# Kernel optimization log

Measured on AMD Instinct MI355X. Metric: run time of the kernel, lower is better.

The kernel has to match this reference:

```python
import jax, jax.numpy as jnp
import numpy as np

D_MODEL = 1024
N_HEAD = 16
D_HEAD = 64  # scale uses d_head even though heads are never split in this module
HD = N_HEAD * D_HEAD  # 1024
LN_EPS = 1e-5


def setup_inputs() -> dict:
    key = jax.random.key(0)
    ks = jax.random.split(key, 12)
    B, S = 8, 2048
    s = 0.02
    return {
        "q": jax.random.normal(ks[0], (B, S, D_MODEL), jnp.float32),
        "k": jax.random.normal(ks[1], (B, S, D_MODEL), jnp.float32),
        "v": jax.random.normal(ks[2], (B, S, D_MODEL), jnp.float32),
        "Wq": jax.random.normal(ks[3], (HD, D_MODEL), jnp.float32) * s,
        "Wk": jax.random.normal(ks[4], (HD, D_MODEL), jnp.float32) * s,
        "bk": jax.random.normal(ks[5], (HD,), jnp.float32) * s,
        "Wv": jax.random.normal(ks[6], (HD, D_MODEL), jnp.float32) * s,
        "bv": jax.random.normal(ks[7], (HD,), jnp.float32) * s,
        "Wo": jax.random.normal(ks[8], (D_MODEL, HD), jnp.float32) * s,
        "bo": jax.random.normal(ks[9], (D_MODEL,), jnp.float32) * s,
        "gamma": jnp.ones((D_MODEL,), jnp.float32),
        "beta": jnp.zeros((D_MODEL,), jnp.float32),
    }


def reference(q, k, v, Wq, Wk, bk, Wv, bv, Wo, bo, gamma, beta):
    scale = 1.0 / np.sqrt(D_HEAD).astype(np.float32)
    # projections (q_head has no bias, matching nn.Linear(bias=False))
    qh = jnp.einsum('bsm,hm->bsh', q, Wq) * scale      # [B,S,HD]
    kh = jnp.einsum('bsm,hm->bsh', k, Wk) + bk         # [B,S,HD]
    vh = jnp.einsum('bsm,hm->bsh', v, Wv) + bv         # [B,S,HD]
    # single effective head: full HD contraction (heads never split in source)
    scores = jnp.einsum('bid,bjd->bij', qh, kh)        # [B,Sq,Sk]
    dtype = scores.dtype
    probs = jax.nn.softmax(scores.astype(jnp.float32), axis=-1).astype(dtype)
    attn = jnp.einsum('bij,bjd->bid', probs, vh)       # [B,Sq,HD]
    attn_out = jnp.einsum('bsh,mh->bsm', attn, Wo) + bo
    x = q + attn_out                                   # dropout/drop_path = identity at eval
    mu = jnp.mean(x, axis=-1, keepdims=True)
    var = jnp.mean(jnp.square(x - mu), axis=-1, keepdims=True)
    return (x - mu) * jax.lax.rsqrt(var + LN_EPS) * gamma + beta
```

## Files before the change

kernel.cpp:

```cpp
#include <hip/hip_runtime.h>

typedef unsigned short u16;
typedef __attribute__((ext_vector_type(8))) short bf16x8;
typedef __attribute__((ext_vector_type(4))) float f32x4;

#define DEVINL static __device__ __forceinline__

DEVINL u16 f2bf(float x) {
  unsigned u = __float_as_uint(x);
  unsigned r = (u + 0x7FFFu + ((u >> 16) & 1u)) >> 16;
  return (u16)r;
}
DEVINL float bf2f(u16 h) { return __uint_as_float(((unsigned)h) << 16); }

DEVINL void gload_lds16(const u16* g, u16* l) {
  __builtin_amdgcn_global_load_lds(
      (const __attribute__((address_space(1))) void*)g,
      (__attribute__((address_space(3))) void*)l, 16, 0, 0);
}

DEVINL int swzg(int r, int s) {
  return ((r >> 1) << 3) + ((((r & 1) << 2) | s) ^ ((r >> 1) & 7));
}

DEVINL void stage_half(const u16* gbase, int K, u16* ldst, int tid) {
#pragma unroll
  for (int i = 0; i < 2; i++) {
    int g = i * 512 + tid;
    int p = g >> 3;
    int w = (g & 7) ^ (p & 7);
    int row = p * 2 + (w >> 2);
    int ks = w & 3;
    gload_lds16(gbase + (size_t)row * K + ks * 8, ldst + g * 8);
  }
}

template <bool HAS_BIAS, bool RESID, bool OUT_F32>
__global__ __launch_bounds__(512, 2) void gemm_bt(
    const u16* __restrict__ Ap, const u16* __restrict__ Bp,
    const float* __restrict__ bias, const float* __restrict__ resid,
    void* __restrict__ Cp, int N, int K, long long Az, long long Bz,
    long long Cz, float scale) {
  const int gx = gridDim.x, gy = gridDim.y;
  int lin = blockIdx.x + gx * (blockIdx.y + gy * blockIdx.z);
  const int nwg = gx * gy * gridDim.z;
  if ((nwg & 7) == 0) {
    const int chunk = nwg >> 3;
    lin = (lin & 7) * chunk + (lin >> 3);
  }
  const int bz = lin / (gx * gy);
  const int rem = lin - bz * gx * gy;
  const int m0 = (rem / gx) * 256, n0 = (rem % gx) * 256;

  const int tid = threadIdx.x, lane = tid & 63, wv = tid >> 6;
  const int wr = wv >> 2, wc = wv & 3, lr = lane & 15, lh = lane >> 4;

  __shared__ u16 lds[3 * 16384];

  const u16* A = Ap + (size_t)bz * Az + (size_t)m0 * K;
  const u16* B = Bp + (size_t)bz * Bz + (size_t)n0 * K;

  f32x4 acc[8][4] = {};
  const int nt = K >> 5;

  stage_half(A, K, &lds[0], tid);
  stage_half(B, K, &lds[8192], tid);
  stage_half(A + 32, K, &lds[16384], tid);
  stage_half(B + 32, K, &lds[16384 + 8192], tid);
  asm volatile("s_waitcnt vmcnt(4)" ::: "memory");
  __builtin_amdgcn_s_barrier();

  int d = 0;
  for (int t = 0; t < nt; ++t) {
    const u16* la = &lds[d * 16384];
    const u16* lb = la + 8192;
    int dn = d + 2;
    if (dn >= 3) dn -= 3;
    const bool doPre = (t + 2) < nt;

    bf16x8 bfv[4], af[4];
#pragma unroll
    for (int n = 0; n < 4; n++) {
      int row = wc * 64 + n * 16 + lr;
      bfv[n] = *(const bf16x8*)&lb[swzg(row, lh) * 8];
    }
#pragma unroll
    for (int m = 0; m < 4; m++) {
      int row = wr * 128 + m * 16 + lr;
      af[m] = *(const bf16x8*)&la[swzg(row, lh) * 8];
    }
    if (doPre) stage_half(A + (size_t)(t + 2) * 32, K, &lds[dn * 16384], tid);
    __builtin_amdgcn_s_setprio(1);
#pragma unroll
    for (int m = 0; m < 4; m++)
#pragma unroll
      for (int n = 0; n < 4; n++)
        acc[m][n] = __builtin_amdgcn_mfma_f32_16x16x32_bf16(af[m], bfv[n],
                                                            acc[m][n], 0, 0, 0);
    __builtin_amdgcn_s_setprio(0);

#pragma unroll
    for (int m = 0; m < 4; m++) {
      int row = wr * 128 + (m + 4) * 16 + lr;
      af[m] = *(const bf16x8*)&la[swzg(row, lh) * 8];
    }
    if (doPre)
      stage_half(B + (size_t)(t + 2) * 32, K, &lds[dn * 16384 + 8192], tid);
    __builtin_amdgcn_s_setprio(1);
#pragma unroll
    for (int m = 0; m < 4; m++)
#pragma unroll
      for (int n = 0; n < 4; n++)
        acc[m + 4][n] = __builtin_amdgcn_mfma_f32_16x16x32_bf16(
            af[m], bfv[n], acc[m + 4][n], 0, 0, 0);
    __builtin_amdgcn_s_setprio(0);

    if (t + 2 < nt)
      asm volatile("s_waitcnt vmcnt(4)" ::: "memory");
    else if (t + 1 < nt)
      asm volatile("s_waitcnt vmcnt(0)" ::: "memory");
    if (t + 1 < nt) __builtin_amdgcn_s_barrier();
    if (++d == 3) d = 0;
  }

  float* Cf = nullptr;
  u16* Ch = nullptr;
  if constexpr (OUT_F32)
    Cf = (float*)Cp + (size_t)bz * Cz;
  else
    Ch = (u16*)Cp + (size_t)bz * Cz;
#pragma unroll
  for (int m = 0; m < 8; m++) {
#pragma unroll
    for (int j = 0; j < 4; j++) {
      int row = m0 + wr * 128 + m * 16 + lh * 4 + j;
#pragma unroll
      for (int n = 0; n < 4; n++) {
        int col = n0 + wc * 64 + n * 16 + lr;
        float val = acc[m][n][j] * scale;
        if constexpr (HAS_BIAS) val += bias[col];
        if constexpr (RESID) val += resid[(size_t)row * N + col];
        if constexpr (OUT_F32)
          Cf[(size_t)row * N + col] = val;
        else
          Ch[(size_t)row * N + col] = f2bf(val);
      }
    }
  }
}

__global__ __launch_bounds__(256) void cvt8(const float* __restrict__ in,
                                            u16* __restrict__ out) {
  const size_t i = ((size_t)blockIdx.x * 256 + threadIdx.x) * 8;
  f32x4 a = *(const f32x4*)&in[i];
  f32x4 b = *(const f32x4*)&in[i + 4];
  bf16x8 h;
#pragma unroll
  for (int u = 0; u < 4; u++) h[u] = (short)f2bf(a[u]);
#pragma unroll
  for (int u = 0; u < 4; u++) h[4 + u] = (short)f2bf(b[u]);
  *(bf16x8*)&out[i] = h;
}

__global__ __launch_bounds__(256) void transpose_bf16(const u16* __restrict__ in,
                                                      u16* __restrict__ out,
                                                      int R, int C) {
  const int z = blockIdx.z;
  const u16* I = in + (size_t)z * R * C;
  u16* O = out + (size_t)z * R * C;
  __shared__ u16 t[64][72];
  const int r0 = blockIdx.y * 64, c0 = blockIdx.x * 64;
  const int tid = threadIdx.x;
#pragma unroll
  for (int i = 0; i < 2; i++) {
    int e = (i * 256 + tid) * 8;
    int r = e >> 6, c = e & 63;
    bf16x8 v = *(const bf16x8*)&I[(size_t)(r0 + r) * C + c0 + c];
#pragma unroll
    for (int u = 0; u < 8; u++) t[r][c + u] = (u16)v[u];
  }
  __syncthreads();
#pragma unroll
  for (int i = 0; i < 2; i++) {
    int e = (i * 256 + tid) * 8;
    int orow = e >> 6, oc = e & 63;
    bf16x8 v;
#pragma unroll
    for (int u = 0; u < 8; u++) v[u] = (short)t[oc + u][orow];
    *(bf16x8*)&O[(size_t)(c0 + orow) * R + r0 + oc] = v;
  }
}

__global__ __launch_bounds__(256) void softmax_rows(u16* __restrict__ p) {
  const size_t base = (size_t)blockIdx.x * 2048;
  const int tid = threadIdx.x, lane = tid & 63, wv = tid >> 6;
  bf16x8 v = *(const bf16x8*)&p[base + tid * 8];
  float f[8];
#pragma unroll
  for (int u = 0; u < 8; u++) f[u] = bf2f((u16)v[u]);
  float mx = f[0];
#pragma unroll
  for (int u = 1; u < 8; u++) mx = fmaxf(mx, f[u]);
#pragma unroll
  for (int o = 32; o; o >>= 1) mx = fmaxf(mx, __shfl_xor(mx, o, 64));
  __shared__ float rm[4], rs[4];
  if (lane == 0) rm[wv] = mx;
  __syncthreads();
  mx = fmaxf(fmaxf(rm[0], rm[1]), fmaxf(rm[2], rm[3]));
  float s = 0.f, e[8];
#pragma unroll
  for (int u = 0; u < 8; u++) {
    e[u] = __expf(f[u] - mx);
    s += e[u];
  }
#pragma unroll
  for (int o = 32; o; o >>= 1) s += __shfl_xor(s, o, 64);
  if (lane == 0) rs[wv] = s;
  __syncthreads();
  s = rs[0] + rs[1] + rs[2] + rs[3];
  float inv = 1.f / s;
  bf16x8 o8;
#pragma unroll
  for (int u = 0; u < 8; u++) o8[u] = (short)f2bf(e[u] * inv);
  *(bf16x8*)&p[base + tid * 8] = o8;
}

__global__ __launch_bounds__(256) void ln_rows(const float* __restrict__ x,
                                               const float* __restrict__ gamma,
                                               const float* __restrict__ beta,
                                               float* __restrict__ out) {
  const size_t base = (size_t)blockIdx.x * 1024;
  const int tid = threadIdx.x, lane = tid & 63, wv = tid >> 6;
  f32x4 v = *(const f32x4*)&x[base + tid * 4];
  float s = v[0] + v[1] + v[2] + v[3];
  float q = v[0] * v[0] + v[1] * v[1] + v[2] * v[2] + v[3] * v[3];
#pragma unroll
  for (int o = 32; o; o >>= 1) {
    s += __shfl_xor(s, o, 64);
    q += __shfl_xor(q, o, 64);
  }
  __shared__ float rs[4], rq[4];
  if (lane == 0) {
    rs[wv] = s;
    rq[wv] = q;
  }
  __syncthreads();
  s = rs[0] + rs[1] + rs[2] + rs[3];
  q = rq[0] + rq[1] + rq[2] + rq[3];
  float mean = s * (1.f / 1024.f);
  float var = q * (1.f / 1024.f) - mean * mean;
  float rstd = rsqrtf(var + 1e-5f);
  f32x4 g = *(const f32x4*)&gamma[tid * 4];
  f32x4 b = *(const f32x4*)&beta[tid * 4];
  f32x4 o;
#pragma unroll
  for (int u = 0; u < 4; u++) o[u] = (v[u] - mean) * rstd * g[u] + b[u];
  *(f32x4*)&out[base + tid * 4] = o;
}

extern "C" void kernel_launch(void* const* d_in, const int* in_sizes, int n_in,
                              void* d_out, int out_size, void* d_ws,
                              size_t ws_size, hipStream_t stream) {
  (void)in_sizes; (void)n_in; (void)out_size; (void)ws_size;
  const float* q = (const float*)d_in[0];
  const float* k = (const float*)d_in[1];
  const float* v = (const float*)d_in[2];
  const float* Wq = (const float*)d_in[3];
  const float* Wk = (const float*)d_in[4];
  const float* bk = (const float*)d_in[5];
  const float* Wv = (const float*)d_in[6];
  const float* bv = (const float*)d_in[7];
  const float* Wo = (const float*)d_in[8];
  const float* bo = (const float*)d_in[9];
  const float* gamma = (const float*)d_in[10];
  const float* beta = (const float*)d_in[11];
  float* out = (float*)d_out;

  char* ws = (char*)d_ws;
  const size_t SZ_QKV = (size_t)16384 * 1024 * 2;
  u16* qh = (u16*)(ws);
  u16* kh = (u16*)(ws + SZ_QKV);
  u16* vh = (u16*)(ws + 2 * SZ_QKV);
  u16* vhT = (u16*)(ws + 3 * SZ_QKV);
  u16* probs = (u16*)(ws + 4 * SZ_QKV);
  u16* qkvb = probs;
  float* xbuf = (float*)(ws + 4 * SZ_QKV);
  u16* attn = qh;
  u16* Wqb = (u16*)(ws + 4 * SZ_QKV + (size_t)67108864);
  u16* Wkb = Wqb + 1048576;
  u16* Wvb = Wkb + 1048576;
  u16* Wob = Wvb + 1048576;

  cvt8<<<512, 256, 0, stream>>>(Wq, Wqb);
  cvt8<<<512, 256, 0, stream>>>(Wk, Wkb);
  cvt8<<<512, 256, 0, stream>>>(Wv, Wvb);
  cvt8<<<512, 256, 0, stream>>>(Wo, Wob);

  dim3 gp(4, 64, 1);
  cvt8<<<8192, 256, 0, stream>>>(q, qkvb);
  gemm_bt<false, false, false><<<gp, 512, 0, stream>>>(
      qkvb, Wqb, nullptr, nullptr, qh, 1024, 1024, 0, 0, 0, 0.125f);
  cvt8<<<8192, 256, 0, stream>>>(k, qkvb);
  gemm_bt<true, false, false><<<gp, 512, 0, stream>>>(
      qkvb, Wkb, bk, nullptr, kh, 1024, 1024, 0, 0, 0, 1.0f);
  cvt8<<<8192, 256, 0, stream>>>(v, qkvb);
  gemm_bt<true, false, false><<<gp, 512, 0, stream>>>(
      qkvb, Wvb, bv, nullptr, vh, 1024, 1024, 0, 0, 0, 1.0f);

  transpose_bf16<<<dim3(16, 32, 8), 256, 0, stream>>>(vh, vhT, 2048, 1024);

  gemm_bt<false, false, false><<<dim3(8, 8, 8), 512, 0, stream>>>(
      qh, kh, nullptr, nullptr, probs, 2048, 1024, 2097152LL, 2097152LL,
      4194304LL, 1.0f);

  softmax_rows<<<16384, 256, 0, stream>>>(probs);

  gemm_bt<false, false, false><<<dim3(4, 8, 8), 512, 0, stream>>>(
      probs, vhT, nullptr, nullptr, attn, 1024, 2048, 4194304LL, 2097152LL,
      2097152LL, 1.0f);

  gemm_bt<true, true, true><<<dim3(4, 64, 1), 512, 0, stream>>>(
      attn, Wob, bo, q, xbuf, 1024, 1024, 0, 0, 0, 1.0f);

  ln_rows<<<16384, 256, 0, stream>>>(xbuf, gamma, beta, out);
}
```

Before: 433.5 us.

## Fuse fp32-to-bf16 input conversion and V transpose into projection GEMMs

The Q/K/V projection GEMMs now read fp32 activations directly and convert them to bf16 while staging into LDS, so the separate cvt8 passes over the three 64MB inputs are gone. The V projection writes its output already transposed, which removes the transpose kernel and the intermediate vh buffer. The four weight conversions are merged into one launch. In exchange, the A-operand prefetch now goes through registers with a synchronous convert and store rather than async global-to-LDS loads, and the transposed epilogue does scattered 8-byte stores, both of which may weaken the pipelining inside the GEMM.

After: 414.7 us. 4.3% less time.

```diff
diff --git a/kernel.cpp b/kernel.cpp
--- a/kernel.cpp
+++ b/kernel.cpp
@@ -2,6 +2,7 @@
 
 typedef unsigned short u16;
 typedef __attribute__((ext_vector_type(8))) short bf16x8;
+typedef __attribute__((ext_vector_type(4))) short bf16x4;
 typedef __attribute__((ext_vector_type(4))) float f32x4;
 
 #define DEVINL static __device__ __forceinline__
@@ -22,22 +23,25 @@
 DEVINL int swzg(int r, int s) {
   return ((r >> 1) << 3) + ((((r & 1) << 2) | s) ^ ((r >> 1) & 7));
 }
+DEVINL void g2rk(int g, int& row, int& ks) {
+  int p = g >> 3, w = (g & 7) ^ (p & 7);
+  row = p * 2 + (w >> 2);
+  ks = w & 3;
+}
 
 DEVINL void stage_half(const u16* gbase, int K, u16* ldst, int tid) {
 #pragma unroll
   for (int i = 0; i < 2; i++) {
     int g = i * 512 + tid;
-    int p = g >> 3;
-    int w = (g & 7) ^ (p & 7);
-    int row = p * 2 + (w >> 2);
-    int ks = w & 3;
+    int row, ks;
+    g2rk(g, row, ks);
     gload_lds16(gbase + (size_t)row * K + ks * 8, ldst + g * 8);
   }
 }
 
-template <bool HAS_BIAS, bool RESID, bool OUT_F32>
+template <bool A_F32, bool HAS_BIAS, bool RESID, bool OUT_F32, bool TRANSV>
 __global__ __launch_bounds__(512, 2) void gemm_bt(
-    const u16* __restrict__ Ap, const u16* __restrict__ Bp,
+    const void* __restrict__ Ap_, const u16* __restrict__ Bp,
     const float* __restrict__ bias, const float* __restrict__ resid,
     void* __restrict__ Cp, int N, int K, long long Az, long long Bz,
     long long Cz, float scale) {
@@ -57,17 +61,46 @@
 
   __shared__ u16 lds[3 * 16384];
 
-  const u16* A = Ap + (size_t)bz * Az + (size_t)m0 * K;
+  const u16* A16 = nullptr;
+  const float* A32 = nullptr;
+  if constexpr (A_F32)
+    A32 = (const float*)Ap_ + (size_t)bz * Az + (size_t)m0 * K;
+  else
+    A16 = (const u16*)Ap_ + (size_t)bz * Az + (size_t)m0 * K;
   const u16* B = Bp + (size_t)bz * Bz + (size_t)n0 * K;
 
   f32x4 acc[8][4] = {};
   const int nt = K >> 5;
 
-  stage_half(A, K, &lds[0], tid);
-  stage_half(B, K, &lds[8192], tid);
-  stage_half(A + 32, K, &lds[16384], tid);
-  stage_half(B + 32, K, &lds[16384 + 8192], tid);
-  asm volatile("s_waitcnt vmcnt(4)" ::: "memory");
+  if constexpr (A_F32) {
+#pragma unroll
+    for (int t = 0; t < 2; t++) {
+      u16* dstA = &lds[t * 16384];
+#pragma unroll
+      for (int i = 0; i < 2; i++) {
+        int g = i * 512 + tid, row, ks;
+        g2rk(g, row, ks);
+        const float* src = A32 + (size_t)row * K + t * 32 + ks * 8;
+        f32x4 a = *(const f32x4*)src;
+        f32x4 b = *(const f32x4*)(src + 4);
+        bf16x8 h;
+#pragma unroll
+        for (int u = 0; u < 4; u++) {
+          h[u] = (short)f2bf(a[u]);
+          h[4 + u] = (short)f2bf(b[u]);
+        }
+        *(bf16x8*)&dstA[g * 8] = h;
+      }
+      stage_half(B + t * 32, K, &lds[t * 16384 + 8192], tid);
+    }
+    asm volatile("s_waitcnt vmcnt(2) lgkmcnt(0)" ::: "memory");
+  } else {
+    stage_half(A16, K, &lds[0], tid);
+    stage_half(B, K, &lds[8192], tid);
+    stage_half(A16 + 32, K, &lds[16384], tid);
+    stage_half(B + 32, K, &lds[16384 + 8192], tid);
+    asm volatile("s_waitcnt vmcnt(4)" ::: "memory");
+  }
   __builtin_amdgcn_s_barrier();
 
   int d = 0;
@@ -89,7 +122,18 @@
       int row = wr * 128 + m * 16 + lr;
       af[m] = *(const bf16x8*)&la[swzg(row, lh) * 8];
     }
-    if (doPre) stage_half(A + (size_t)(t + 2) * 32, K, &lds[dn * 16384], tid);
+    f32x4 pre0, pre1;
+    if constexpr (A_F32) {
+      if (doPre) {
+        int row, ks;
+        g2rk(tid, row, ks);
+        const float* src = A32 + (size_t)row * K + (t + 2) * 32 + ks * 8;
+        pre0 = *(const f32x4*)src;
+        pre1 = *(const f32x4*)(src + 4);
+      }
+    } else {
+      if (doPre) stage_half(A16 + (size_t)(t + 2) * 32, K, &lds[dn * 16384], tid);
+    }
     __builtin_amdgcn_s_setprio(1);
 #pragma unroll
     for (int m = 0; m < 4; m++)
@@ -104,8 +148,31 @@
       int row = wr * 128 + (m + 4) * 16 + lr;
       af[m] = *(const bf16x8*)&la[swzg(row, lh) * 8];
     }
-    if (doPre)
-      stage_half(B + (size_t)(t + 2) * 32, K, &lds[dn * 16384 + 8192], tid);
+    if (doPre) stage_half(B + (size_t)(t + 2) * 32, K, &lds[dn * 16384 + 8192], tid);
+    if constexpr (A_F32) {
+      if (doPre) {
+        u16* dstA = &lds[dn * 16384];
+        bf16x8 h0;
+#pragma unroll
+        for (int u = 0; u < 4; u++) {
+          h0[u] = (short)f2bf(pre0[u]);
+          h0[4 + u] = (short)f2bf(pre1[u]);
+        }
+        *(bf16x8*)&dstA[tid * 8] = h0;
+        int g = 512 + tid, row, ks;
+        g2rk(g, row, ks);
+        const float* src = A32 + (size_t)row * K + (t + 2) * 32 + ks * 8;
+        f32x4 a = *(const f32x4*)src;
+        f32x4 b = *(const f32x4*)(src + 4);
+        bf16x8 h1;
+#pragma unroll
+        for (int u = 0; u < 4; u++) {
+          h1[u] = (short)f2bf(a[u]);
+          h1[4 + u] = (short)f2bf(b[u]);
+        }
+        *(bf16x8*)&dstA[g * 8] = h1;
+      }
+    }
     __builtin_amdgcn_s_setprio(1);
 #pragma unroll
     for (int m = 0; m < 4; m++)
@@ -115,80 +182,85 @@
             af[m], bfv[n], acc[m + 4][n], 0, 0, 0);
     __builtin_amdgcn_s_setprio(0);
 
-    if (t + 2 < nt)
-      asm volatile("s_waitcnt vmcnt(4)" ::: "memory");
-    else if (t + 1 < nt)
-      asm volatile("s_waitcnt vmcnt(0)" ::: "memory");
+    if constexpr (A_F32) {
+      if (doPre)
+        asm volatile("s_waitcnt vmcnt(2) lgkmcnt(0)" ::: "memory");
+      else if (t + 1 < nt)
+        asm volatile("s_waitcnt vmcnt(0) lgkmcnt(0)" ::: "memory");
+    } else {
+      if (doPre)
+        asm volatile("s_waitcnt vmcnt(4)" ::: "memory");
+      else if (t + 1 < nt)
+        asm volatile("s_waitcnt vmcnt(0)" ::: "memory");
+    }
     if (t + 1 < nt) __builtin_amdgcn_s_barrier();
     if (++d == 3) d = 0;
   }
 
-  float* Cf = nullptr;
-  u16* Ch = nullptr;
-  if constexpr (OUT_F32)
-    Cf = (float*)Cp + (size_t)bz * Cz;
-  else
-    Ch = (u16*)Cp + (size_t)bz * Cz;
-#pragma unroll
-  for (int m = 0; m < 8; m++) {
-#pragma unroll
-    for (int j = 0; j < 4; j++) {
-      int row = m0 + wr * 128 + m * 16 + lh * 4 + j;
+  if constexpr (TRANSV) {
+    u16* Ch = (u16*)Cp;
+#pragma unroll
+    for (int m = 0; m < 8; m++) {
+      int row0 = m0 + wr * 128 + m * 16 + lh * 4;
+      int b = row0 >> 11, s = row0 & 2047;
 #pragma unroll
       for (int n = 0; n < 4; n++) {
         int col = n0 + wc * 64 + n * 16 + lr;
-        float val = acc[m][n][j] * scale;
-        if constexpr (HAS_BIAS) val += bias[col];
-        if constexpr (RESID) val += resid[(size_t)row * N + col];
-        if constexpr (OUT_F32)
-          Cf[(size_t)row * N + col] = val;
-        else
-          Ch[(size_t)row * N + col] = f2bf(val);
-      }
-    }
-  }
-}
-
-__global__ __launch_bounds__(256) void cvt8(const float* __restrict__ in,
-                                            u16* __restrict__ out) {
-  const size_t i = ((size_t)blockIdx.x * 256 + threadIdx.x) * 8;
+        bf16x4 pack;
+#pragma unroll
+        for (int j = 0; j < 4; j++) {
+          float val = acc[m][n][j] * scale;
+          if constexpr (HAS_BIAS) val += bias[col];
+          pack[j] = (short)f2bf(val);
+        }
+        *(bf16x4*)&Ch[((size_t)b << 21) + ((size_t)col << 11) + s] = pack;
+      }
+    }
+  } else {
+    float* Cf = nullptr;
+    u16* Ch = nullptr;
+    if constexpr (OUT_F32)
+      Cf = (float*)Cp + (size_t)bz * Cz;
+    else
+      Ch = (u16*)Cp + (size_t)bz * Cz;
+#pragma unroll
+    for (int m = 0; m < 8; m++) {
+#pragma unroll
+      for (int j = 0; j < 4; j++) {
+        int row = m0 + wr * 128 + m * 16 + lh * 4 + j;
+#pragma unroll
+        for (int n = 0; n < 4; n++) {
+          int col = n0 + wc * 64 + n * 16 + lr;
+          float val = acc[m][n][j] * scale;
+          if constexpr (HAS_BIAS) val += bias[col];
+          if constexpr (RESID) val += resid[(size_t)row * N + col];
+          if constexpr (OUT_F32)
+            Cf[(size_t)row * N + col] = val;
+          else
+            Ch[(size_t)row * N + col] = f2bf(val);
+        }
+      }
+    }
+  }
+}
+
+__global__ __launch_bounds__(256) void cvt8w(const float* __restrict__ w0,
+                                             const float* __restrict__ w1,
+                                             const float* __restrict__ w2,
+                                             const float* __restrict__ w3,
+                                             u16* __restrict__ out) {
+  const int wsel = blockIdx.x >> 9;
+  const float* in = wsel == 0 ? w0 : wsel == 1 ? w1 : wsel == 2 ? w2 : w3;
+  const size_t i = ((size_t)(blockIdx.x & 511) * 256 + threadIdx.x) * 8;
   f32x4 a = *(const f32x4*)&in[i];
   f32x4 b = *(const f32x4*)&in[i + 4];
   bf16x8 h;
 #pragma unroll
-  for (int u = 0; u < 4; u++) h[u] = (short)f2bf(a[u]);
-#pragma unroll
-  for (int u = 0; u < 4; u++) h[4 + u] = (short)f2bf(b[u]);
-  *(bf16x8*)&out[i] = h;
-}
-
-__global__ __launch_bounds__(256) void transpose_bf16(const u16* __restrict__ in,
-                                                      u16* __restrict__ out,
-                                                      int R, int C) {
-  const int z = blockIdx.z;
-  const u16* I = in + (size_t)z * R * C;
-  u16* O = out + (size_t)z * R * C;
-  __shared__ u16 t[64][72];
-  const int r0 = blockIdx.y * 64, c0 = blockIdx.x * 64;
-  const int tid = threadIdx.x;
-#pragma unroll
-  for (int i = 0; i < 2; i++) {
-    int e = (i * 256 + tid) * 8;
-    int r = e >> 6, c = e & 63;
-    bf16x8 v = *(const bf16x8*)&I[(size_t)(r0 + r) * C + c0 + c];
-#pragma unroll
-    for (int u = 0; u < 8; u++) t[r][c + u] = (u16)v[u];
-  }
-  __syncthreads();
-#pragma unroll
-  for (int i = 0; i < 2; i++) {
-    int e = (i * 256 + tid) * 8;
-    int orow = e >> 6, oc = e & 63;
-    bf16x8 v;
-#pragma unroll
-    for (int u = 0; u < 8; u++) v[u] = (short)t[oc + u][orow];
-    *(bf16x8*)&O[(size_t)(c0 + orow) * R + r0 + oc] = v;
-  }
+  for (int u = 0; u < 4; u++) {
+    h[u] = (short)f2bf(a[u]);
+    h[4 + u] = (short)f2bf(b[u]);
+  }
+  *(bf16x8*)&out[(size_t)wsel * 1048576 + i] = h;
 }
 
 __global__ __launch_bounds__(256) void softmax_rows(u16* __restrict__ p) {
@@ -280,10 +352,8 @@
   const size_t SZ_QKV = (size_t)16384 * 1024 * 2;
   u16* qh = (u16*)(ws);
   u16* kh = (u16*)(ws + SZ_QKV);
-  u16* vh = (u16*)(ws + 2 * SZ_QKV);
   u16* vhT = (u16*)(ws + 3 * SZ_QKV);
   u16* probs = (u16*)(ws + 4 * SZ_QKV);
-  u16* qkvb = probs;
   float* xbuf = (float*)(ws + 4 * SZ_QKV);
   u16* attn = qh;
   u16* Wqb = (u16*)(ws + 4 * SZ_QKV + (size_t)67108864);
@@ -291,35 +361,27 @@
   u16* Wvb = Wkb + 1048576;
   u16* Wob = Wvb + 1048576;
 
-  cvt8<<<512, 256, 0, stream>>>(Wq, Wqb);
-  cvt8<<<512, 256, 0, stream>>>(Wk, Wkb);
-  cvt8<<<512, 256, 0, stream>>>(Wv, Wvb);
-  cvt8<<<512, 256, 0, stream>>>(Wo, Wob);
+  cvt8w<<<2048, 256, 0, stream>>>(Wq, Wk, Wv, Wo, Wqb);
 
   dim3 gp(4, 64, 1);
-  cvt8<<<8192, 256, 0, stream>>>(q, qkvb);
-  gemm_bt<false, false, false><<<gp, 512, 0, stream>>>(
-      qkvb, Wqb, nullptr, nullptr, qh, 1024, 1024, 0, 0, 0, 0.125f);
-  cvt8<<<8192, 256, 0, stream>>>(k, qkvb);
-  gemm_bt<true, false, false><<<gp, 512, 0, stream>>>(
-      qkvb, Wkb, bk, nullptr, kh, 1024, 1024, 0, 0, 0, 1.0f);
-  cvt8<<<8192, 256, 0, stream>>>(v, qkvb);
-  gemm_bt<true, false, false><<<gp, 512, 0, stream>>>(
-      qkvb, Wvb, bv, nullptr, vh, 1024, 1024, 0, 0, 0, 1.0f);
-
-  transpose_bf16<<<dim3(16, 32, 8), 256, 0, stream>>>(vh, vhT, 2048, 1024);
-
-  gemm_bt<false, false, false><<<dim3(8, 8, 8), 512, 0, stream>>>(
+  gemm_bt<true, false, false, false, false><<<gp, 512, 0, stream>>>(
+      q, Wqb, nullptr, nullptr, qh, 1024, 1024, 0, 0, 0, 0.125f);
+  gemm_bt<true, true, false, false, false><<<gp, 512, 0, stream>>>(
+      k, Wkb, bk, nullptr, kh, 1024, 1024, 0, 0, 0, 1.0f);
+  gemm_bt<true, true, false, false, true><<<gp, 512, 0, stream>>>(
+      v, Wvb, bv, nullptr, vhT, 1024, 1024, 0, 0, 0, 1.0f);
+
+  gemm_bt<false, false, false, false, false><<<dim3(8, 8, 8), 512, 0, stream>>>(
       qh, kh, nullptr, nullptr, probs, 2048, 1024, 2097152LL, 2097152LL,
       4194304LL, 1.0f);
 
   softmax_rows<<<16384, 256, 0, stream>>>(probs);
 
-  gemm_bt<false, false, false><<<dim3(4, 8, 8), 512, 0, stream>>>(
+  gemm_bt<false, false, false, false, false><<<dim3(4, 8, 8), 512, 0, stream>>>(
       probs, vhT, nullptr, nullptr, attn, 1024, 2048, 4194304LL, 2097152LL,
       2097152LL, 1.0f);
 
-  gemm_bt<true, true, true><<<dim3(4, 64, 1), 512, 0, stream>>>(
+  gemm_bt<false, true, true, true, false><<<dim3(4, 64, 1), 512, 0, stream>>>(
       attn, Wob, bo, q, xbuf, 1024, 1024, 0, 0, 0, 1.0f);
 
   ln_rows<<<16384, 256, 0, stream>>>(xbuf, gamma, beta, out);
```
